# Performance work log

Hardware: AMD Instinct MI355X
Metric: run time of the kernel (lower is better)

The kernel has to match this reference:

```python
import jax, jax.numpy as jnp
import numpy as np

N_NODES = 100000
N_EDGES = 3200000
D_IN = 128


def setup_inputs() -> dict:
    key = jax.random.key(0)
    k1, k2, k3, k4 = jax.random.split(key, 4)
    x = jax.random.normal(k1, (N_NODES, D_IN), dtype=jnp.float32)
    edge_index = jax.random.randint(k2, (2, N_EDGES), 0, N_NODES, dtype=jnp.int64)
    W1 = jax.random.normal(k3, (D_IN, 16), dtype=jnp.float32) * (1.0 / np.sqrt(D_IN))
    b1 = jnp.zeros((16,), dtype=jnp.float32)
    W2 = jax.random.normal(k4, (16, 2), dtype=jnp.float32) * (1.0 / np.sqrt(16))
    b2 = jnp.zeros((2,), dtype=jnp.float32)
    return {"x": x, "edge_index": edge_index, "W1": W1, "b1": b1, "W2": W2, "b2": b2}


def _gcn_norm(edge_index, n_nodes):
    # Add self-loops, then symmetric degree normalization (PyG gcn_norm).
    loops = jnp.arange(n_nodes, dtype=edge_index.dtype)
    row = jnp.concatenate([edge_index[0], loops])  # source
    col = jnp.concatenate([edge_index[1], loops])  # target
    ones = jnp.ones(row.shape[0], dtype=jnp.float32)
    deg = jax.ops.segment_sum(ones, col, num_segments=n_nodes)
    dis = jnp.where(deg > 0, jax.lax.rsqrt(deg), 0.0)  # deg^{-1/2}
    norm = dis[row] * dis[col]  # [E+N]
    return row, col, norm


def _gcn_conv(x, row, col, norm, W, b, n_nodes):
    h = x @ W  # transform first (PyG order): [N, out]
    msgs = h[row] * norm[:, None]  # gather from source, scale
    agg = jax.ops.segment_sum(msgs, col, num_segments=n_nodes)  # scatter-add to target
    return agg + b


def reference(x, edge_index, W1, b1, W2, b2):
    n = x.shape[0]
    row, col, norm = _gcn_norm(edge_index, n)
    h = _gcn_conv(x, row, col, norm, W1, b1, n)
    h = jax.nn.relu(h)
    h = _gcn_conv(h, row, col, norm, W2, b2, n)
    return jax.nn.log_softmax(h, axis=1)
```

## Files before the change

kernel.cpp:

```cpp
#include <hip/hip_runtime.h>
#include <hip/hip_fp16.h>

#define DIN 128
#define BSH 7
#define BSIZE 128
#define NBMAX 800
#define CAP 4480
#define CHUNK 6656
#define EPT 13
#define PB 512
#define HR 128
#define XSTR 136
#define PZ 0xAAAAAAAAu

typedef _Float16 half8_t __attribute__((ext_vector_type(8)));
typedef _Float16 half4_t __attribute__((ext_vector_type(4)));
typedef float f32x4_t __attribute__((ext_vector_type(4)));

struct PlaceSmem {
    int pk[CHUNK];
    unsigned short bkid[CHUNK];
    int lcnt[NBMAX], lstart[NBMAX], gofs[NBMAX], lcur[NBMAX];
    int sst[16];
};
struct HSmem {
    _Float16 xh[HR * XSTR];
};
union __align__(16) MegaSmem {
    PlaceSmem p;
    HSmem h;
};

__global__ __launch_bounds__(PB, 6) void mega_kernel(const int* __restrict__ row,
                                                     const int* __restrict__ col,
                                                     const float* __restrict__ x,
                                                     const float* __restrict__ W1,
                                                     unsigned* __restrict__ cur,
                                                     int* __restrict__ sp,
                                                     __half* __restrict__ hp,
                                                     int E, int N, int NB, int PBLKS) {
    __shared__ MegaSmem sm;
    int t = threadIdx.x;
    int bid = blockIdx.x;

    if (bid < PBLKS) {
        int e0 = bid * CHUNK;
        int cnt = min(CHUNK, E - e0);
        bool full = (cnt == CHUNK);
        for (int i = t; i < NBMAX; i += PB) { sm.p.lcnt[i] = 0; sm.p.lcur[i] = 0; }
        __syncthreads();
        int cv[EPT], rv[EPT];
        if (full) {
            #pragma unroll
            for (int k = 0; k < EPT; k++) cv[k] = col[e0 + t + k * PB];
            #pragma unroll
            for (int k = 0; k < EPT; k++) rv[k] = row[e0 + t + k * PB];
            #pragma unroll
            for (int k = 0; k < EPT; k++) atomicAdd(&sm.p.lcnt[cv[k] >> BSH], 1);
        } else {
            for (int i = t; i < cnt; i += PB)
                atomicAdd(&sm.p.lcnt[col[e0 + i] >> BSH], 1);
        }
        __syncthreads();
        int b2i = t * 2;
        int v0 = (b2i + 0 < NBMAX) ? sm.p.lcnt[b2i + 0] : 0;
        int v1 = (b2i + 1 < NBMAX) ? sm.p.lcnt[b2i + 1] : 0;
        unsigned g0 = 0, g1 = 0;
        if (b2i + 0 < NB && v0) g0 = atomicAdd(&cur[b2i + 0], (unsigned)v0) - PZ;
        if (b2i + 1 < NB && v1) g1 = atomicAdd(&cur[b2i + 1], (unsigned)v1) - PZ;
        int tot = v0 + v1;
        int lane = t & 63, w = t >> 6;
        int sc = tot;
        #pragma unroll
        for (int d = 1; d < 64; d <<= 1) {
            int up = __shfl_up(sc, d);
            if (lane >= d) sc += up;
        }
        if (lane == 63) sm.p.sst[w] = sc;
        __syncthreads();
        if (t < 64) {
            int v = (lane < 8) ? sm.p.sst[lane] : 0;
            #pragma unroll
            for (int d = 1; d < 8; d <<= 1) {
                int up = __shfl_up(v, d);
                if (lane >= d) v += up;
            }
            if (lane < 8) sm.p.sst[8 + lane] = v;
        }
        __syncthreads();
        int wpre = (w > 0) ? sm.p.sst[8 + w - 1] : 0;
        int ex = sc + wpre - tot;
        if (b2i + 0 < NBMAX) sm.p.lstart[b2i + 0] = ex;
        if (b2i + 1 < NBMAX) sm.p.lstart[b2i + 1] = ex + v0;
        if (b2i + 0 < NB) sm.p.gofs[b2i + 0] = (b2i + 0) * CAP + (int)g0 - ex;
        if (b2i + 1 < NB) sm.p.gofs[b2i + 1] = (b2i + 1) * CAP + (int)g1 - (ex + v0);
        __syncthreads();
        if (full) {
            #pragma unroll
            for (int k = 0; k < EPT; k++) {
                int cc = cv[k];
                int b  = cc >> BSH;
                int rk = atomicAdd(&sm.p.lcur[b], 1);
                int pos = sm.p.lstart[b] + rk;
                sm.p.pk[pos]   = ((cc & (BSIZE - 1)) << 17) | rv[k];
                sm.p.bkid[pos] = (unsigned short)b;
            }
            __syncthreads();
            #pragma unroll
            for (int k = 0; k < EPT; k++) {
                int i = t + k * PB;
                sp[sm.p.gofs[sm.p.bkid[i]] + i] = sm.p.pk[i];
            }
        } else {
            for (int i = t; i < cnt; i += PB) {
                int r  = row[e0 + i];
                int cc = col[e0 + i];
                int b  = cc >> BSH;
                int rk = atomicAdd(&sm.p.lcur[b], 1);
                int pos = sm.p.lstart[b] + rk;
                sm.p.pk[pos]   = ((cc & (BSIZE - 1)) << 17) | r;
                sm.p.bkid[pos] = (unsigned short)b;
            }
            __syncthreads();
            for (int i = t; i < cnt; i += PB)
                sp[sm.p.gofs[sm.p.bkid[i]] + i] = sm.p.pk[i];
        }
    } else {
        int base = (bid - PBLKS) * HR;
        _Float16* xh = sm.h.xh;
        int nrow = min(HR, N - base);
        int lane = t & 63, w = t >> 6;
        int cl = lane & 15;
        int kg = (lane >> 4) * 8;
        half8_t bf[4];
        #pragma unroll
        for (int s = 0; s < 4; s++) {
            #pragma unroll
            for (int i = 0; i < 8; i++)
                bf[s][i] = (_Float16)W1[(s * 32 + kg + i) * 16 + cl];
        }
        #pragma unroll
        for (int q = 0; q < 8; q++) {
            int idx = q * 512 + t;
            int r = idx >> 5, c4 = idx & 31;
            float4 v = make_float4(0.f, 0.f, 0.f, 0.f);
            if (r < nrow) v = *(const float4*)(x + (size_t)(base + r) * DIN + c4 * 4);
            half4_t h4;
            h4[0] = (_Float16)v.x; h4[1] = (_Float16)v.y;
            h4[2] = (_Float16)v.z; h4[3] = (_Float16)v.w;
            *(half4_t*)(xh + r * XSTR + c4 * 4) = h4;
        }
        __syncthreads();
        int mb = w * 16;
        const _Float16* xr = xh + (mb + cl) * XSTR;
        f32x4_t acc = {0.f, 0.f, 0.f, 0.f};
        #pragma unroll
        for (int s = 0; s < 4; s++) {
            half8_t af = *(const half8_t*)(xr + kg + s * 32);
            acc = __builtin_amdgcn_mfma_f32_16x16x32_f16(af, bf[s], acc, 0, 0, 0);
        }
        int m0 = mb + (lane >> 4) * 4;
        #pragma unroll
        for (int r = 0; r < 4; r++) {
            int n = base + m0 + r;
            if (n < N) hp[(size_t)n * 16 + cl] = __float2half((float)acc[r]);
        }
    }
}

__global__ __launch_bounds__(256) void dscale_kernel(const int* __restrict__ sp,
                                                     const unsigned* __restrict__ cur,
                                                     __half* __restrict__ hp, int N) {
    __shared__ int lcnt[BSIZE];
    __shared__ float disl[BSIZE];
    int b = blockIdx.x;
    int t = threadIdx.x;
    int cntb = (int)(cur[b] - PZ);
    const int* src = sp + (size_t)b * CAP;
    if (t < BSIZE) lcnt[t] = 0;
    __syncthreads();
    int n4 = cntb >> 2;
    const int4* src4 = (const int4*)src;
    #pragma unroll 2
    for (int i = t; i < n4; i += 256) {
        int4 v = src4[i];
        atomicAdd(&lcnt[v.x >> 17], 1);
        atomicAdd(&lcnt[v.y >> 17], 1);
        atomicAdd(&lcnt[v.z >> 17], 1);
        atomicAdd(&lcnt[v.w >> 17], 1);
    }
    for (int i = (n4 << 2) + t; i < cntb; i += 256)
        atomicAdd(&lcnt[src[i] >> 17], 1);
    __syncthreads();
    if (t < BSIZE) disl[t] = rsqrtf((float)lcnt[t] + 1.0f);
    __syncthreads();
    int r = t >> 1, part = t & 1;
    int gt = b * BSIZE + r;
    if (gt < N) {
        uint4* p = (uint4*)(hp + (size_t)gt * 16) + part;
        uint4 v = *p;
        __half2* h2 = (__half2*)&v;
        float dv = disl[r];
        #pragma unroll
        for (int q = 0; q < 4; q++) {
            float2 f = __half22float2(h2[q]);
            f.x *= dv; f.y *= dv;
            h2[q] = __float22half2_rn(f);
        }
        *p = v;
    }
}

__global__ __launch_bounds__(512) void bsg1_kernel(const int* __restrict__ sp,
                                                   const unsigned* __restrict__ cur,
                                                   const __half2* __restrict__ hp2,
                                                   const float* __restrict__ b1,
                                                   const float* __restrict__ W2,
                                                   int* __restrict__ srt2,
                                                   int* __restrict__ off,
                                                   float* __restrict__ gp, int N) {
    __shared__ int ss[CAP];
    __shared__ int lcnt[BSIZE], lstart[BSIZE], lcur[BSIZE];
    __shared__ int stot[2];
    int B = blockIdx.x;
    int t = threadIdx.x;
    int cntb = (int)(cur[B] - PZ);
    const int* reg = sp + (size_t)B * CAP;
    if (t < BSIZE) { lcnt[t] = 0; lcur[t] = 0; }
    __syncthreads();
    int rc[9];
    #pragma unroll
    for (int k = 0; k < 9; k++) {
        int i = k * 512 + t;
        rc[k] = (i < cntb) ? reg[i] : -1;
    }
    #pragma unroll
    for (int k = 0; k < 9; k++)
        if (rc[k] >= 0) atomicAdd(&lcnt[rc[k] >> 17], 1);
    __syncthreads();
    int lane = t & 63, w = t >> 6;
    int v = (t < BSIZE) ? lcnt[t] : 0;
    int sc = v;
    #pragma unroll
    for (int d = 1; d < 64; d <<= 1) {
        int up = __shfl_up(sc, d);
        if (lane >= d) sc += up;
    }
    if (t < BSIZE && lane == 63) stot[w] = sc;
    __syncthreads();
    if (t < BSIZE) lstart[t] = sc - v + ((w == 1) ? stot[0] : 0);
    __syncthreads();
    #pragma unroll
    for (int k = 0; k < 9; k++) {
        int vv = rc[k];
        if (vv >= 0) {
            int lc = vv >> 17;
            int rk = atomicAdd(&lcur[lc], 1);
            ss[lstart[lc] + rk] = vv & 0x1FFFF;
        }
    }
    __syncthreads();
    for (int i = t; i < cntb; i += 512) srt2[(size_t)B * CAP + i] = ss[i];
    if (t < BSIZE) {
        off[B * (BSIZE + 1) + t] = B * CAP + lstart[t];
    } else if (t == BSIZE) {
        off[B * (BSIZE + 1) + BSIZE] = B * CAP + cntb;
    }
    int k2  = t & 7;
    int ltg = t >> 3;
    #pragma unroll
    for (int r2 = 0; r2 < 2; r2++) {
        int lt = r2 * 64 + ltg;
        int gt = B * BSIZE + lt;
        if (gt < N) {
            int j0 = lstart[lt];
            int j1 = j0 + lcnt[lt];
            float2 acc0 = __half22float2(hp2[(size_t)gt * 8 + k2]);
            float2 acc1 = make_float2(0.f, 0.f);
            float2 acc2 = make_float2(0.f, 0.f);
            float2 acc3 = make_float2(0.f, 0.f);
            int j = j0;
            for (; j + 3 < j1; j += 4) {
                int r0 = ss[j + 0], r1 = ss[j + 1], r2i = ss[j + 2], r3 = ss[j + 3];
                float2 h0 = __half22float2(hp2[(size_t)r0 * 8 + k2]);
                float2 h1 = __half22float2(hp2[(size_t)r1 * 8 + k2]);
                float2 h2 = __half22float2(hp2[(size_t)r2i * 8 + k2]);
                float2 h3 = __half22float2(hp2[(size_t)r3 * 8 + k2]);
                acc0.x += h0.x; acc0.y += h0.y;
                acc1.x += h1.x; acc1.y += h1.y;
                acc2.x += h2.x; acc2.y += h2.y;
                acc3.x += h3.x; acc3.y += h3.y;
            }
            for (; j < j1; j++) {
                int r = ss[j];
                float2 hv = __half22float2(hp2[(size_t)r * 8 + k2]);
                acc0.x += hv.x; acc0.y += hv.y;
            }
            float2 acc = make_float2(acc0.x + acc1.x + acc2.x + acc3.x,
                                     acc0.y + acc1.y + acc2.y + acc3.y);
            float d = rsqrtf((float)lcnt[lt] + 1.0f);
            int k0 = k2 * 2;
            float v0 = fmaxf(fmaf(acc.x, d, b1[k0 + 0]), 0.0f);
            float v1 = fmaxf(fmaf(acc.y, d, b1[k0 + 1]), 0.0f);
            float p0 = v0 * W2[k0 * 2 + 0] + v1 * W2[k0 * 2 + 2];
            float p1 = v0 * W2[k0 * 2 + 1] + v1 * W2[k0 * 2 + 3];
            p0 += __shfl_xor(p0, 1); p1 += __shfl_xor(p1, 1);
            p0 += __shfl_xor(p0, 2); p1 += __shfl_xor(p1, 2);
            p0 += __shfl_xor(p0, 4); p1 += __shfl_xor(p1, 4);
            if (k2 == 0) *(float2*)(gp + (size_t)gt * 2) = make_float2(p0 * d, p1 * d);
        }
    }
}

__global__ __launch_bounds__(256) void g2_kernel(const int* __restrict__ srt2,
                                                 const int* __restrict__ off,
                                                 const float* __restrict__ gp,
                                                 const float* __restrict__ b2,
                                                 float* __restrict__ out, int N) {
    int t = blockIdx.x * 256 + threadIdx.x;
    int c    = t >> 3;
    int slot = t & 7;
    if (c >= N) return;
    int idx = (c >> 7) * (BSIZE + 1) + (c & 127);
    int j0 = off[idx];
    int j1 = off[idx + 1];
    float a0 = 0.0f, a1v = 0.0f;
    float c0 = 0.0f, c1v = 0.0f;
    int j = j0 + slot;
    for (; j + 24 < j1; j += 32) {
        int r0 = srt2[j];
        int r1 = srt2[j + 8];
        int r2 = srt2[j + 16];
        int r3 = srt2[j + 24];
        float2 g0 = *(const float2*)(gp + (size_t)r0 * 2);
        float2 g1 = *(const float2*)(gp + (size_t)r1 * 2);
        float2 g2 = *(const float2*)(gp + (size_t)r2 * 2);
        float2 g3 = *(const float2*)(gp + (size_t)r3 * 2);
        a0  += g0.x + g2.x;  a1v += g0.y + g2.y;
        c0  += g1.x + g3.x;  c1v += g1.y + g3.y;
    }
    for (; j < j1; j += 8) {
        int r = srt2[j];
        float2 gv = *(const float2*)(gp + (size_t)r * 2);
        a0  += gv.x;
        a1v += gv.y;
    }
    a0 += c0; a1v += c1v;
    a0 += __shfl_xor(a0, 1); a1v += __shfl_xor(a1v, 1);
    a0 += __shfl_xor(a0, 2); a1v += __shfl_xor(a1v, 2);
    a0 += __shfl_xor(a0, 4); a1v += __shfl_xor(a1v, 4);
    if (slot == 0) {
        float2 self = *(const float2*)(gp + (size_t)c * 2);
        float d = rsqrtf((float)(j1 - j0) + 1.0f);
        float o0 = (a0  + self.x) * d + b2[0];
        float o1 = (a1v + self.y) * d + b2[1];
        float m = fmaxf(o0, o1);
        float lse = m + logf(expf(o0 - m) + expf(o1 - m));
        *(float2*)(out + (size_t)c * 2) = make_float2(o0 - lse, o1 - lse);
    }
}

extern "C" void kernel_launch(void* const* d_in, const int* in_sizes, int n_in,
                              void* d_out, int out_size, void* d_ws, size_t ws_size,
                              hipStream_t stream) {
    const float* x  = (const float*)d_in[0];
    const int*   ei = (const int*)d_in[1];
    const float* W1 = (const float*)d_in[2];
    const float* b1 = (const float*)d_in[3];
    const float* W2 = (const float*)d_in[4];
    const float* b2 = (const float*)d_in[5];
    float* out = (float*)d_out;

    const int N = in_sizes[0] / DIN;
    const int E = in_sizes[1] / 2;
    const int* row = ei;
    const int* col = ei + E;
    const int NB    = (N + BSIZE - 1) / BSIZE;
    const int PBLKS = (E + CHUNK - 1) / CHUNK;
    const int HBLKS = (N + HR - 1) / HR;

    unsigned* cur  = (unsigned*)d_ws;
    int*      off  = (int*)(cur + NBMAX);
    int*      sp   = off + (size_t)NBMAX * (BSIZE + 1);
    int*      srt2 = sp + (size_t)NBMAX * CAP;
    __half*   hp   = (__half*)(srt2 + (size_t)NBMAX * CAP);
    float*    gp   = (float*)(hp + (size_t)N * 16);

    mega_kernel  <<<PBLKS + HBLKS, PB, 0, stream>>>(row, col, x, W1, cur, sp, hp, E, N, NB, PBLKS);
    dscale_kernel<<<NB, 256, 0, stream>>>(sp, cur, hp, N);
    bsg1_kernel  <<<NB, 512, 0, stream>>>(sp, cur, (const __half2*)hp, b1, W2, srt2, off, gp, N);
    g2_kernel    <<<(int)(((size_t)N * 8 + 255) / 256), 256, 0, stream>>>(srt2, off, gp, b2, out, N);
}
```

Baseline: 178.4 us.

## Drop dscale pass; compute deg^-1/2 in sort kernel and apply per-edge in gather

Removes the separate dscale kernel that re-counted degrees and rewrote the fp16 hidden features scaled by the source degree. The sort kernel now writes a per-node dis array, and a new g1 kernel reloads the sorted sources and applies dis[src] through an FMA for each gathered edge. This saves one histogram pass and a read-modify-write of hp, but adds a random 4-byte dis load per edge, an extra kernel boundary, and a global round trip of the sorted list between sort and gather.

```diff
diff --git a/kernel.cpp b/kernel.cpp
--- a/kernel.cpp
+++ b/kernel.cpp
@@ -168,57 +168,11 @@
     }
 }
 
-__global__ __launch_bounds__(256) void dscale_kernel(const int* __restrict__ sp,
-                                                     const unsigned* __restrict__ cur,
-                                                     __half* __restrict__ hp, int N) {
-    __shared__ int lcnt[BSIZE];
-    __shared__ float disl[BSIZE];
-    int b = blockIdx.x;
-    int t = threadIdx.x;
-    int cntb = (int)(cur[b] - PZ);
-    const int* src = sp + (size_t)b * CAP;
-    if (t < BSIZE) lcnt[t] = 0;
-    __syncthreads();
-    int n4 = cntb >> 2;
-    const int4* src4 = (const int4*)src;
-    #pragma unroll 2
-    for (int i = t; i < n4; i += 256) {
-        int4 v = src4[i];
-        atomicAdd(&lcnt[v.x >> 17], 1);
-        atomicAdd(&lcnt[v.y >> 17], 1);
-        atomicAdd(&lcnt[v.z >> 17], 1);
-        atomicAdd(&lcnt[v.w >> 17], 1);
-    }
-    for (int i = (n4 << 2) + t; i < cntb; i += 256)
-        atomicAdd(&lcnt[src[i] >> 17], 1);
-    __syncthreads();
-    if (t < BSIZE) disl[t] = rsqrtf((float)lcnt[t] + 1.0f);
-    __syncthreads();
-    int r = t >> 1, part = t & 1;
-    int gt = b * BSIZE + r;
-    if (gt < N) {
-        uint4* p = (uint4*)(hp + (size_t)gt * 16) + part;
-        uint4 v = *p;
-        __half2* h2 = (__half2*)&v;
-        float dv = disl[r];
-        #pragma unroll
-        for (int q = 0; q < 4; q++) {
-            float2 f = __half22float2(h2[q]);
-            f.x *= dv; f.y *= dv;
-            h2[q] = __float22half2_rn(f);
-        }
-        *p = v;
-    }
-}
-
-__global__ __launch_bounds__(512) void bsg1_kernel(const int* __restrict__ sp,
+__global__ __launch_bounds__(512) void sort_kernel(const int* __restrict__ sp,
                                                    const unsigned* __restrict__ cur,
-                                                   const __half2* __restrict__ hp2,
-                                                   const float* __restrict__ b1,
-                                                   const float* __restrict__ W2,
                                                    int* __restrict__ srt2,
                                                    int* __restrict__ off,
-                                                   float* __restrict__ gp, int N) {
+                                                   float* __restrict__ dis, int N) {
     __shared__ int ss[CAP];
     __shared__ int lcnt[BSIZE], lstart[BSIZE], lcur[BSIZE];
     __shared__ int stot[2];
@@ -263,9 +217,27 @@
     for (int i = t; i < cntb; i += 512) srt2[(size_t)B * CAP + i] = ss[i];
     if (t < BSIZE) {
         off[B * (BSIZE + 1) + t] = B * CAP + lstart[t];
+        int gt = B * BSIZE + t;
+        if (gt < N) dis[gt] = rsqrtf((float)lcnt[t] + 1.0f);
     } else if (t == BSIZE) {
         off[B * (BSIZE + 1) + BSIZE] = B * CAP + cntb;
     }
+}
+
+__global__ __launch_bounds__(512) void g1_kernel(const int* __restrict__ srt2,
+                                                 const int* __restrict__ off,
+                                                 const unsigned* __restrict__ cur,
+                                                 const __half2* __restrict__ hp2,
+                                                 const float* __restrict__ dis,
+                                                 const float* __restrict__ b1,
+                                                 const float* __restrict__ W2,
+                                                 float* __restrict__ gp, int N) {
+    __shared__ int ss[CAP];
+    int B = blockIdx.x;
+    int t = threadIdx.x;
+    int cntb = (int)(cur[B] - PZ);
+    for (int i = t; i < cntb; i += 512) ss[i] = srt2[(size_t)B * CAP + i];
+    __syncthreads();
     int k2  = t & 7;
     int ltg = t >> 3;
     #pragma unroll
@@ -273,41 +245,46 @@
         int lt = r2 * 64 + ltg;
         int gt = B * BSIZE + lt;
         if (gt < N) {
-            int j0 = lstart[lt];
-            int j1 = j0 + lcnt[lt];
-            float2 acc0 = __half22float2(hp2[(size_t)gt * 8 + k2]);
+            int o0 = off[B * (BSIZE + 1) + lt];
+            int o1 = off[B * (BSIZE + 1) + lt + 1];
+            int j0 = o0 - B * CAP;
+            int j1 = o1 - B * CAP;
+            float dgt = dis[gt];
+            float2 sv = __half22float2(hp2[(size_t)gt * 8 + k2]);
+            float2 acc0 = make_float2(sv.x * dgt, sv.y * dgt);
             float2 acc1 = make_float2(0.f, 0.f);
             float2 acc2 = make_float2(0.f, 0.f);
             float2 acc3 = make_float2(0.f, 0.f);
             int j = j0;
             for (; j + 3 < j1; j += 4) {
                 int r0 = ss[j + 0], r1 = ss[j + 1], r2i = ss[j + 2], r3 = ss[j + 3];
+                float d0 = dis[r0], d1 = dis[r1], d2 = dis[r2i], d3 = dis[r3];
                 float2 h0 = __half22float2(hp2[(size_t)r0 * 8 + k2]);
                 float2 h1 = __half22float2(hp2[(size_t)r1 * 8 + k2]);
                 float2 h2 = __half22float2(hp2[(size_t)r2i * 8 + k2]);
                 float2 h3 = __half22float2(hp2[(size_t)r3 * 8 + k2]);
-                acc0.x += h0.x; acc0.y += h0.y;
-                acc1.x += h1.x; acc1.y += h1.y;
-                acc2.x += h2.x; acc2.y += h2.y;
-                acc3.x += h3.x; acc3.y += h3.y;
+                acc0.x = fmaf(h0.x, d0, acc0.x); acc0.y = fmaf(h0.y, d0, acc0.y);
+                acc1.x = fmaf(h1.x, d1, acc1.x); acc1.y = fmaf(h1.y, d1, acc1.y);
+                acc2.x = fmaf(h2.x, d2, acc2.x); acc2.y = fmaf(h2.y, d2, acc2.y);
+                acc3.x = fmaf(h3.x, d3, acc3.x); acc3.y = fmaf(h3.y, d3, acc3.y);
             }
             for (; j < j1; j++) {
                 int r = ss[j];
+                float dr = dis[r];
                 float2 hv = __half22float2(hp2[(size_t)r * 8 + k2]);
-                acc0.x += hv.x; acc0.y += hv.y;
+                acc0.x = fmaf(hv.x, dr, acc0.x); acc0.y = fmaf(hv.y, dr, acc0.y);
             }
             float2 acc = make_float2(acc0.x + acc1.x + acc2.x + acc3.x,
                                      acc0.y + acc1.y + acc2.y + acc3.y);
-            float d = rsqrtf((float)lcnt[lt] + 1.0f);
             int k0 = k2 * 2;
-            float v0 = fmaxf(fmaf(acc.x, d, b1[k0 + 0]), 0.0f);
-            float v1 = fmaxf(fmaf(acc.y, d, b1[k0 + 1]), 0.0f);
+            float v0 = fmaxf(fmaf(acc.x, dgt, b1[k0 + 0]), 0.0f);
+            float v1 = fmaxf(fmaf(acc.y, dgt, b1[k0 + 1]), 0.0f);
             float p0 = v0 * W2[k0 * 2 + 0] + v1 * W2[k0 * 2 + 2];
             float p1 = v0 * W2[k0 * 2 + 1] + v1 * W2[k0 * 2 + 3];
             p0 += __shfl_xor(p0, 1); p1 += __shfl_xor(p1, 1);
             p0 += __shfl_xor(p0, 2); p1 += __shfl_xor(p1, 2);
             p0 += __shfl_xor(p0, 4); p1 += __shfl_xor(p1, 4);
-            if (k2 == 0) *(float2*)(gp + (size_t)gt * 2) = make_float2(p0 * d, p1 * d);
+            if (k2 == 0) *(float2*)(gp + (size_t)gt * 2) = make_float2(p0 * dgt, p1 * dgt);
         }
     }
 }
@@ -385,9 +362,10 @@
     int*      srt2 = sp + (size_t)NBMAX * CAP;
     __half*   hp   = (__half*)(srt2 + (size_t)NBMAX * CAP);
     float*    gp   = (float*)(hp + (size_t)N * 16);
-
-    mega_kernel  <<<PBLKS + HBLKS, PB, 0, stream>>>(row, col, x, W1, cur, sp, hp, E, N, NB, PBLKS);
-    dscale_kernel<<<NB, 256, 0, stream>>>(sp, cur, hp, N);
-    bsg1_kernel  <<<NB, 512, 0, stream>>>(sp, cur, (const __half2*)hp, b1, W2, srt2, off, gp, N);
-    g2_kernel    <<<(int)(((size_t)N * 8 + 255) / 256), 256, 0, stream>>>(srt2, off, gp, b2, out, N);
-}
+    float*    dis  = gp + (size_t)N * 2;
+
+    mega_kernel <<<PBLKS + HBLKS, PB, 0, stream>>>(row, col, x, W1, cur, sp, hp, E, N, NB, PBLKS);
+    sort_kernel <<<NB, 512, 0, stream>>>(sp, cur, srt2, off, dis, N);
+    g1_kernel   <<<NB, 512, 0, stream>>>(srt2, off, cur, (const __half2*)hp, dis, b1, W2, gp, N);
+    g2_kernel   <<<(int)(((size_t)N * 8 + 255) / 256), 256, 0, stream>>>(srt2, off, gp, b2, out, N);
+}
```

Result: slower. 193.6 us (+8.6%).

## Split fused placement/transform megakernel into separate place and h kernels

Applied to the files above, without the earlier changes.

The heterogeneous mega kernel, which ran edge bucket placement blocks and the x@W1 MFMA transform blocks in one launch, is split into two kernels launched back to back on the same stream. Each kernel now allocates only its own shared memory, and the h kernel gets its own launch bounds allowing higher occupancy. The trade is losing the concurrency between the two independent phases and adding one more launch and kernel boundary.

```diff
diff --git a/kernel.cpp b/kernel.cpp
--- a/kernel.cpp
+++ b/kernel.cpp
@@ -17,154 +17,147 @@
 typedef _Float16 half4_t __attribute__((ext_vector_type(4)));
 typedef float f32x4_t __attribute__((ext_vector_type(4)));
 
+
 struct PlaceSmem {
     int pk[CHUNK];
     unsigned short bkid[CHUNK];
     int lcnt[NBMAX], lstart[NBMAX], gofs[NBMAX], lcur[NBMAX];
     int sst[16];
 };
-struct HSmem {
-    _Float16 xh[HR * XSTR];
-};
-union __align__(16) MegaSmem {
-    PlaceSmem p;
-    HSmem h;
-};
-
-__global__ __launch_bounds__(PB, 6) void mega_kernel(const int* __restrict__ row,
-                                                     const int* __restrict__ col,
-                                                     const float* __restrict__ x,
-                                                     const float* __restrict__ W1,
-                                                     unsigned* __restrict__ cur,
-                                                     int* __restrict__ sp,
-                                                     __half* __restrict__ hp,
-                                                     int E, int N, int NB, int PBLKS) {
-    __shared__ MegaSmem sm;
+
+__global__ __launch_bounds__(PB, 6) void place_kernel(const int* __restrict__ row,
+                                                      const int* __restrict__ col,
+                                                      unsigned* __restrict__ cur,
+                                                      int* __restrict__ sp,
+                                                      int E, int NB) {
+    __shared__ PlaceSmem sm;
     int t = threadIdx.x;
     int bid = blockIdx.x;
-
-    if (bid < PBLKS) {
-        int e0 = bid * CHUNK;
-        int cnt = min(CHUNK, E - e0);
-        bool full = (cnt == CHUNK);
-        for (int i = t; i < NBMAX; i += PB) { sm.p.lcnt[i] = 0; sm.p.lcur[i] = 0; }
+    int e0 = bid * CHUNK;
+    int cnt = min(CHUNK, E - e0);
+    bool full = (cnt == CHUNK);
+    for (int i = t; i < NBMAX; i += PB) { sm.lcnt[i] = 0; sm.lcur[i] = 0; }
+    __syncthreads();
+    int cv[EPT], rv[EPT];
+    if (full) {
+        #pragma unroll
+        for (int k = 0; k < EPT; k++) cv[k] = col[e0 + t + k * PB];
+        #pragma unroll
+        for (int k = 0; k < EPT; k++) rv[k] = row[e0 + t + k * PB];
+        #pragma unroll
+        for (int k = 0; k < EPT; k++) atomicAdd(&sm.lcnt[cv[k] >> BSH], 1);
+    } else {
+        for (int i = t; i < cnt; i += PB)
+            atomicAdd(&sm.lcnt[col[e0 + i] >> BSH], 1);
+    }
+    __syncthreads();
+    int b2i = t * 2;
+    int v0 = (b2i + 0 < NBMAX) ? sm.lcnt[b2i + 0] : 0;
+    int v1 = (b2i + 1 < NBMAX) ? sm.lcnt[b2i + 1] : 0;
+    unsigned g0 = 0, g1 = 0;
+    if (b2i + 0 < NB && v0) g0 = atomicAdd(&cur[b2i + 0], (unsigned)v0) - PZ;
+    if (b2i + 1 < NB && v1) g1 = atomicAdd(&cur[b2i + 1], (unsigned)v1) - PZ;
+    int tot = v0 + v1;
+    int lane = t & 63, w = t >> 6;
+    int sc = tot;
+    #pragma unroll
+    for (int d = 1; d < 64; d <<= 1) {
+        int up = __shfl_up(sc, d);
+        if (lane >= d) sc += up;
+    }
+    if (lane == 63) sm.sst[w] = sc;
+    __syncthreads();
+    if (t < 64) {
+        int v = (lane < 8) ? sm.sst[lane] : 0;
+        #pragma unroll
+        for (int d = 1; d < 8; d <<= 1) {
+            int up = __shfl_up(v, d);
+            if (lane >= d) v += up;
+        }
+        if (lane < 8) sm.sst[8 + lane] = v;
+    }
+    __syncthreads();
+    int wpre = (w > 0) ? sm.sst[8 + w - 1] : 0;
+    int ex = sc + wpre - tot;
+    if (b2i + 0 < NBMAX) sm.lstart[b2i + 0] = ex;
+    if (b2i + 1 < NBMAX) sm.lstart[b2i + 1] = ex + v0;
+    if (b2i + 0 < NB) sm.gofs[b2i + 0] = (b2i + 0) * CAP + (int)g0 - ex;
+    if (b2i + 1 < NB) sm.gofs[b2i + 1] = (b2i + 1) * CAP + (int)g1 - (ex + v0);
+    __syncthreads();
+    if (full) {
+        #pragma unroll
+        for (int k = 0; k < EPT; k++) {
+            int cc = cv[k];
+            int b  = cc >> BSH;
+            int rk = atomicAdd(&sm.lcur[b], 1);
+            int pos = sm.lstart[b] + rk;
+            sm.pk[pos]   = ((cc & (BSIZE - 1)) << 17) | rv[k];
+            sm.bkid[pos] = (unsigned short)b;
+        }
         __syncthreads();
-        int cv[EPT], rv[EPT];
-        if (full) {
-            #pragma unroll
-            for (int k = 0; k < EPT; k++) cv[k] = col[e0 + t + k * PB];
-            #pragma unroll
-            for (int k = 0; k < EPT; k++) rv[k] = row[e0 + t + k * PB];
-            #pragma unroll
-            for (int k = 0; k < EPT; k++) atomicAdd(&sm.p.lcnt[cv[k] >> BSH], 1);
-        } else {
-            for (int i = t; i < cnt; i += PB)
-                atomicAdd(&sm.p.lcnt[col[e0 + i] >> BSH], 1);
+        #pragma unroll
+        for (int k = 0; k < EPT; k++) {
+            int i = t + k * PB;
+            sp[sm.gofs[sm.bkid[i]] + i] = sm.pk[i];
+        }
+    } else {
+        for (int i = t; i < cnt; i += PB) {
+            int r  = row[e0 + i];
+            int cc = col[e0 + i];
+            int b  = cc >> BSH;
+            int rk = atomicAdd(&sm.lcur[b], 1);
+            int pos = sm.lstart[b] + rk;
+            sm.pk[pos]   = ((cc & (BSIZE - 1)) << 17) | r;
+            sm.bkid[pos] = (unsigned short)b;
         }
         __syncthreads();
-        int b2i = t * 2;
-        int v0 = (b2i + 0 < NBMAX) ? sm.p.lcnt[b2i + 0] : 0;
-        int v1 = (b2i + 1 < NBMAX) ? sm.p.lcnt[b2i + 1] : 0;
-        unsigned g0 = 0, g1 = 0;
-        if (b2i + 0 < NB && v0) g0 = atomicAdd(&cur[b2i + 0], (unsigned)v0) - PZ;
-        if (b2i + 1 < NB && v1) g1 = atomicAdd(&cur[b2i + 1], (unsigned)v1) - PZ;
-        int tot = v0 + v1;
-        int lane = t & 63, w = t >> 6;
-        int sc = tot;
-        #pragma unroll
-        for (int d = 1; d < 64; d <<= 1) {
-            int up = __shfl_up(sc, d);
-            if (lane >= d) sc += up;
-        }
-        if (lane == 63) sm.p.sst[w] = sc;
-        __syncthreads();
-        if (t < 64) {
-            int v = (lane < 8) ? sm.p.sst[lane] : 0;
-            #pragma unroll
-            for (int d = 1; d < 8; d <<= 1) {
-                int up = __shfl_up(v, d);
-                if (lane >= d) v += up;
-            }
-            if (lane < 8) sm.p.sst[8 + lane] = v;
-        }
-        __syncthreads();
-        int wpre = (w > 0) ? sm.p.sst[8 + w - 1] : 0;
-        int ex = sc + wpre - tot;
-        if (b2i + 0 < NBMAX) sm.p.lstart[b2i + 0] = ex;
-        if (b2i + 1 < NBMAX) sm.p.lstart[b2i + 1] = ex + v0;
-        if (b2i + 0 < NB) sm.p.gofs[b2i + 0] = (b2i + 0) * CAP + (int)g0 - ex;
-        if (b2i + 1 < NB) sm.p.gofs[b2i + 1] = (b2i + 1) * CAP + (int)g1 - (ex + v0);
-        __syncthreads();
-        if (full) {
-            #pragma unroll
-            for (int k = 0; k < EPT; k++) {
-                int cc = cv[k];
-                int b  = cc >> BSH;
-                int rk = atomicAdd(&sm.p.lcur[b], 1);
-                int pos = sm.p.lstart[b] + rk;
-                sm.p.pk[pos]   = ((cc & (BSIZE - 1)) << 17) | rv[k];
-                sm.p.bkid[pos] = (unsigned short)b;
-            }
-            __syncthreads();
-            #pragma unroll
-            for (int k = 0; k < EPT; k++) {
-                int i = t + k * PB;
-                sp[sm.p.gofs[sm.p.bkid[i]] + i] = sm.p.pk[i];
-            }
-        } else {
-            for (int i = t; i < cnt; i += PB) {
-                int r  = row[e0 + i];
-                int cc = col[e0 + i];
-                int b  = cc >> BSH;
-                int rk = atomicAdd(&sm.p.lcur[b], 1);
-                int pos = sm.p.lstart[b] + rk;
-                sm.p.pk[pos]   = ((cc & (BSIZE - 1)) << 17) | r;
-                sm.p.bkid[pos] = (unsigned short)b;
-            }
-            __syncthreads();
-            for (int i = t; i < cnt; i += PB)
-                sp[sm.p.gofs[sm.p.bkid[i]] + i] = sm.p.pk[i];
-        }
-    } else {
-        int base = (bid - PBLKS) * HR;
-        _Float16* xh = sm.h.xh;
-        int nrow = min(HR, N - base);
-        int lane = t & 63, w = t >> 6;
-        int cl = lane & 15;
-        int kg = (lane >> 4) * 8;
-        half8_t bf[4];
-        #pragma unroll
-        for (int s = 0; s < 4; s++) {
-            #pragma unroll
-            for (int i = 0; i < 8; i++)
-                bf[s][i] = (_Float16)W1[(s * 32 + kg + i) * 16 + cl];
-        }
-        #pragma unroll
-        for (int q = 0; q < 8; q++) {
-            int idx = q * 512 + t;
-            int r = idx >> 5, c4 = idx & 31;
-            float4 v = make_float4(0.f, 0.f, 0.f, 0.f);
-            if (r < nrow) v = *(const float4*)(x + (size_t)(base + r) * DIN + c4 * 4);
-            half4_t h4;
-            h4[0] = (_Float16)v.x; h4[1] = (_Float16)v.y;
-            h4[2] = (_Float16)v.z; h4[3] = (_Float16)v.w;
-            *(half4_t*)(xh + r * XSTR + c4 * 4) = h4;
-        }
-        __syncthreads();
-        int mb = w * 16;
-        const _Float16* xr = xh + (mb + cl) * XSTR;
-        f32x4_t acc = {0.f, 0.f, 0.f, 0.f};
-        #pragma unroll
-        for (int s = 0; s < 4; s++) {
-            half8_t af = *(const half8_t*)(xr + kg + s * 32);
-            acc = __builtin_amdgcn_mfma_f32_16x16x32_f16(af, bf[s], acc, 0, 0, 0);
-        }
-        int m0 = mb + (lane >> 4) * 4;
-        #pragma unroll
-        for (int r = 0; r < 4; r++) {
-            int n = base + m0 + r;
-            if (n < N) hp[(size_t)n * 16 + cl] = __float2half((float)acc[r]);
-        }
+        for (int i = t; i < cnt; i += PB)
+            sp[sm.gofs[sm.bkid[i]] + i] = sm.pk[i];
+    }
+}
+
+__global__ __launch_bounds__(512, 8) void h_kernel(const float* __restrict__ x,
+                                                   const float* __restrict__ W1,
+                                                   __half* __restrict__ hp, int N) {
+    __shared__ _Float16 xh[HR * XSTR];
+    int t = threadIdx.x;
+    int base = blockIdx.x * HR;
+    int nrow = min(HR, N - base);
+    int lane = t & 63, w = t >> 6;
+    int cl = lane & 15;
+    int kg = (lane >> 4) * 8;
+    half8_t bf[4];
+    #pragma unroll
+    for (int s = 0; s < 4; s++) {
+        #pragma unroll
+        for (int i = 0; i < 8; i++)
+            bf[s][i] = (_Float16)W1[(s * 32 + kg + i) * 16 + cl];
+    }
+    #pragma unroll
+    for (int q = 0; q < 8; q++) {
+        int idx = q * 512 + t;
+        int r = idx >> 5, c4 = idx & 31;
+        float4 v = make_float4(0.f, 0.f, 0.f, 0.f);
+        if (r < nrow) v = *(const float4*)(x + (size_t)(base + r) * DIN + c4 * 4);
+        half4_t h4;
+        h4[0] = (_Float16)v.x; h4[1] = (_Float16)v.y;
+        h4[2] = (_Float16)v.z; h4[3] = (_Float16)v.w;
+        *(half4_t*)(xh + r * XSTR + c4 * 4) = h4;
+    }
+    __syncthreads();
+    int mb = w * 16;
+    const _Float16* xr = xh + (mb + cl) * XSTR;
+    f32x4_t acc = {0.f, 0.f, 0.f, 0.f};
+    #pragma unroll
+    for (int s = 0; s < 4; s++) {
+        half8_t af = *(const half8_t*)(xr + kg + s * 32);
+        acc = __builtin_amdgcn_mfma_f32_16x16x32_f16(af, bf[s], acc, 0, 0, 0);
+    }
+    int m0 = mb + (lane >> 4) * 4;
+    #pragma unroll
+    for (int r = 0; r < 4; r++) {
+        int n = base + m0 + r;
+        if (n < N) hp[(size_t)n * 16 + cl] = __float2half((float)acc[r]);
     }
 }
 
@@ -386,7 +379,8 @@
     __half*   hp   = (__half*)(srt2 + (size_t)NBMAX * CAP);
     float*    gp   = (float*)(hp + (size_t)N * 16);
 
-    mega_kernel  <<<PBLKS + HBLKS, PB, 0, stream>>>(row, col, x, W1, cur, sp, hp, E, N, NB, PBLKS);
+    place_kernel <<<PBLKS, PB, 0, stream>>>(row, col, cur, sp, E, NB);
+    h_kernel     <<<HBLKS, 512, 0, stream>>>(x, W1, hp, N);
     dscale_kernel<<<NB, 256, 0, stream>>>(sp, cur, hp, N);
     bsg1_kernel  <<<NB, 512, 0, stream>>>(sp, cur, (const __half2*)hp, b1, W2, srt2, off, gp, N);
     g2_kernel    <<<(int)(((size_t)N * 8 + 255) / 256), 256, 0, stream>>>(srt2, off, gp, b2, out, N);
```

After: 181.9 us. Within noise of the previous version (+2.0%).
